# Kernel optimization log

Measured on AMD Instinct MI355X. Metric: run time of the kernel, lower is better.

The kernel has to match this reference:

```python
import jax, jax.numpy as jnp
import numpy as np

N = 100000      # nodes
E = 1600000     # edges (avg degree 16)
IN, HID, OUT = 128, 32, 64
H = 4           # attention heads in hidden layers

def _p(key, shape, scale=0.1):
    return jax.random.normal(key, shape, dtype=jnp.float32) * scale

def setup_inputs():
    key = jax.random.key(0)
    ks = jax.random.split(key, 16)
    return {
        "x": jax.random.normal(ks[0], (N, IN), dtype=jnp.float32),
        "edge_index": jax.random.randint(ks[1], (2, E), 0, N, dtype=jnp.int32),
        # layer 1: GATConv(IN -> HID, heads=4, concat=True) + BN
        "W1": _p(ks[2], (IN, H * HID)), "as1": _p(ks[3], (H, HID)), "ad1": _p(ks[4], (H, HID)),
        "b1": jnp.zeros((H * HID,), jnp.float32),
        "g1": jnp.ones((H * HID,), jnp.float32), "be1": jnp.zeros((H * HID,), jnp.float32),
        "rm1": _p(ks[5], (H * HID,)), "rv1": jnp.ones((H * HID,), jnp.float32),
        # layer 2: GATConv(H*HID -> HID, heads=4, concat=True) + BN
        "W2": _p(ks[6], (H * HID, H * HID)), "as2": _p(ks[7], (H, HID)), "ad2": _p(ks[8], (H, HID)),
        "b2": jnp.zeros((H * HID,), jnp.float32),
        "g2": jnp.ones((H * HID,), jnp.float32), "be2": jnp.zeros((H * HID,), jnp.float32),
        "rm2": _p(ks[9], (H * HID,)), "rv2": jnp.ones((H * HID,), jnp.float32),
        # layer 3: GATConv(H*HID -> OUT, heads=1, concat=False)
        "W3": _p(ks[10], (H * HID, OUT)), "as3": _p(ks[11], (1, OUT)), "ad3": _p(ks[12], (1, OUT)),
        "b3": jnp.zeros((OUT,), jnp.float32),
    }

def _gat(x, W, a_s, a_d, b, src, dst, heads, ch, concat):
    n = x.shape[0]
    h = (x @ W).reshape(n, heads, ch)                        # [N,H,C]
    e = (h * a_s).sum(-1)[src] + (h * a_d).sum(-1)[dst]      # per-edge logits [E,H]
    e = jax.nn.leaky_relu(e, 0.2)
    m = jax.ops.segment_max(e, dst, num_segments=n)          # segment softmax over dst
    ex = jnp.exp(e - m[dst])
    den = jax.ops.segment_sum(ex, dst, num_segments=n)
    alpha = ex / den[dst]                                    # self loops guarantee den > 0
    out = jax.ops.segment_sum(h[src] * alpha[:, :, None], dst, num_segments=n)
    out = out.reshape(n, heads * ch) if concat else out.mean(axis=1)
    return out + b

def _bn(x, g, b, rm, rv):                                    # BatchNorm1d, eval mode
    return (x - rm) * jax.lax.rsqrt(rv + 1e-5) * g + b

def _forward(x, edge_index, W1, as1, ad1, b1, g1, be1, rm1, rv1,
             W2, as2, ad2, b2, g2, be2, rm2, rv2, W3, as3, ad3, b3):
    n = x.shape[0]
    loop = jnp.arange(n, dtype=edge_index.dtype)             # add self loops (PyG default)
    src = jnp.concatenate([edge_index[0], loop])
    dst = jnp.concatenate([edge_index[1], loop])
    h = _gat(x, W1, as1, ad1, b1, src, dst, H, HID, True)
    h = jax.nn.elu(_bn(h, g1, be1, rm1, rv1))                # dropout = identity (eval)
    h = _gat(h, W2, as2, ad2, b2, src, dst, H, HID, True)
    h = jax.nn.elu(_bn(h, g2, be2, rm2, rv2))
    return _gat(h, W3, as3, ad3, b3, src, dst, 1, OUT, False)

def reference(x, edge_index, W1, as1, ad1, b1, g1, be1, rm1, rv1,
              W2, as2, ad2, b2, g2, be2, rm2, rv2, W3, as3, ad3, b3):
    return _forward(x, edge_index, W1, as1, ad1, b1, g1, be1, rm1, rv1,
                    W2, as2, ad2, b2, g2, be2, rm2, rv2, W3, as3, ad3, b3)
```

## Files before the change

### kernel.cpp

```cpp
#include <hip/hip_runtime.h>
#include <hip/hip_fp16.h>
#include <type_traits>

#define CDIV(a,b) (((a)+(b)-1)/(b))

typedef _Float16 f16x8 __attribute__((ext_vector_type(8)));
typedef float f32x4 __attribute__((ext_vector_type(4)));

__device__ __forceinline__ void wxform(const float* __restrict__ W,
                                       _Float16* __restrict__ Wt, int i, int NOUT) {
  int k = i / NOUT, c = i % NOUT;
  int s = k >> 5, g = (k >> 3) & 3, e = k & 7;
  Wt[(size_t)((s * 4 + g) * NOUT + c) * 8 + e] = (_Float16)W[i];
}
__global__ __launch_bounds__(256) void wprep_all(const float* __restrict__ W1,
                                                 const float* __restrict__ W2,
                                                 const float* __restrict__ W3,
                                                 _Float16* __restrict__ Wt1,
                                                 _Float16* __restrict__ Wt2,
                                                 _Float16* __restrict__ Wt3) {
  int i = blockIdx.x * blockDim.x + threadIdx.x;
  if (i < 128 * 128) { wxform(W1, Wt1, i, 128); wxform(W2, Wt2, i, 128); }
  if (i < 128 * 64)  { wxform(W3, Wt3, i, 64); }
}

template<typename AT>
__device__ __forceinline__ f16x8 load_afrag(const AT* __restrict__ xrow) {
  if constexpr (std::is_same<AT, _Float16>::value) {
    return *reinterpret_cast<const f16x8*>(xrow);
  } else {
    float4 v0 = *reinterpret_cast<const float4*>(xrow);
    float4 v1 = *reinterpret_cast<const float4*>(xrow + 4);
    f16x8 r = {(_Float16)v0.x, (_Float16)v0.y, (_Float16)v0.z, (_Float16)v0.w,
               (_Float16)v1.x, (_Float16)v1.y, (_Float16)v1.z, (_Float16)v1.w};
    return r;
  }
}

template<int NOUT, int HEADS, typename AT>
__global__ __launch_bounds__(256) void gemm_sc(const AT* __restrict__ X,
                                               const _Float16* __restrict__ Wt,
                                               const float* __restrict__ as_,
                                               const float* __restrict__ ad_,
                                               __half* __restrict__ Y,
                                               float* __restrict__ ssrc,
                                               float* __restrict__ sdst, int nrows) {
  constexpr int K = 128;
  constexpr int CT = NOUT / 16;
  constexpr int CH = NOUT / HEADS;
  constexpr int CPH = CH / 16;
  const int wave = threadIdx.x >> 6, lane = threadIdx.x & 63;
  const int g = lane >> 4, r16 = lane & 15;
  const int rt = blockIdx.x * 4 + wave;
  if (rt * 16 >= nrows) return;

  const AT* xrow = X + (size_t)(rt * 16 + r16) * K + g * 8;
  f16x8 a[4];
  #pragma unroll
  for (int s = 0; s < 4; ++s) a[s] = load_afrag(xrow + s * 32);

  f32x4 acc[CT];
  #pragma unroll
  for (int ct = 0; ct < CT; ++ct) acc[ct] = (f32x4){0.f, 0.f, 0.f, 0.f};

  #pragma unroll
  for (int ct = 0; ct < CT; ++ct) {
    #pragma unroll
    for (int s = 0; s < 4; ++s) {
      f16x8 b = *reinterpret_cast<const f16x8*>(&Wt[(size_t)((s * 4 + g) * NOUT + ct * 16 + r16) * 8]);
      acc[ct] = __builtin_amdgcn_mfma_f32_16x16x32_f16(a[s], b, acc[ct], 0, 0, 0);
    }
  }
  const int row0 = rt * 16 + g * 4;
  #pragma unroll
  for (int ct = 0; ct < CT; ++ct) {
    #pragma unroll
    for (int r = 0; r < 4; ++r) {
      Y[(size_t)(row0 + r) * NOUT + ct * 16 + r16] = __float2half_rn(acc[ct][r]);
    }
  }

  float pas[4][HEADS], pad_[4][HEADS];
  #pragma unroll
  for (int r = 0; r < 4; ++r)
    #pragma unroll
    for (int h = 0; h < HEADS; ++h) { pas[r][h] = 0.f; pad_[r][h] = 0.f; }
  #pragma unroll
  for (int h = 0; h < HEADS; ++h) {
    #pragma unroll
    for (int q = 0; q < CPH; ++q) {
      float asv = as_[h * CH + q * 16 + r16];
      float adv = ad_[h * CH + q * 16 + r16];
      #pragma unroll
      for (int r = 0; r < 4; ++r) {
        float av = acc[h * CPH + q][r];
        pas[r][h] += av * asv;
        pad_[r][h] += av * adv;
      }
    }
  }
  #pragma unroll
  for (int off = 1; off < 16; off <<= 1) {
    #pragma unroll
    for (int r = 0; r < 4; ++r)
      #pragma unroll
      for (int h = 0; h < HEADS; ++h) {
        pas[r][h] += __shfl_xor(pas[r][h], off);
        pad_[r][h] += __shfl_xor(pad_[r][h], off);
      }
  }
  #pragma unroll
  for (int h = 0; h < HEADS; ++h) {
    if (r16 == h) {
      #pragma unroll
      for (int r = 0; r < 4; ++r) ssrc[(size_t)(row0 + r) * HEADS + h] = pas[r][h];
    }
    if (r16 == 8 + h) {
      #pragma unroll
      for (int r = 0; r < 4; ++r) sdst[(size_t)(row0 + r) * HEADS + h] = pad_[r][h];
    }
  }
}

__global__ __launch_bounds__(256) void hist_kernel(const int* __restrict__ ei, int E,
                                                   int* __restrict__ deg) {
  int e = blockIdx.x * blockDim.x + threadIdx.x;
  if (e >= E) return;
  atomicAdd(&deg[ei[E + e]], 1);
}

__global__ __launch_bounds__(256) void scan_blocksums(const int* __restrict__ deg,
                                                      int* __restrict__ bsum, int N) {
  __shared__ int red[256];
  int base = blockIdx.x * 1024 + threadIdx.x * 4;
  int s = 0;
  #pragma unroll
  for (int i = 0; i < 4; ++i) { int idx = base + i; if (idx < N) s += deg[idx]; }
  red[threadIdx.x] = s;
  __syncthreads();
  for (int off = 128; off > 0; off >>= 1) {
    if (threadIdx.x < off) red[threadIdx.x] += red[threadIdx.x + off];
    __syncthreads();
  }
  if (threadIdx.x == 0) bsum[blockIdx.x] = red[0];
}

__global__ __launch_bounds__(1024) void scan_bsum(int* __restrict__ bsum, int nb) {
  __shared__ int sh[1024];
  int t = threadIdx.x;
  int v = (t < nb) ? bsum[t] : 0;
  sh[t] = v;
  __syncthreads();
  for (int off = 1; off < 1024; off <<= 1) {
    int tmp = (t >= off) ? sh[t - off] : 0;
    __syncthreads();
    sh[t] += tmp;
    __syncthreads();
  }
  if (t < nb) bsum[t] = sh[t] - v;
}

__global__ __launch_bounds__(256) void scan_final(const int* __restrict__ deg,
                                                  const int* __restrict__ bsum,
                                                  int* __restrict__ rowptr,
                                                  int* __restrict__ cursor, int N) {
  __shared__ int sh[256];
  const int t = threadIdx.x;
  const int base = blockIdx.x * 1024 + t * 4;
  int d[4] = {0, 0, 0, 0};
  #pragma unroll
  for (int i = 0; i < 4; ++i) if (base + i < N) d[i] = deg[base + i];
  int s = d[0] + d[1] + d[2] + d[3];
  sh[t] = s;
  __syncthreads();
  for (int off = 1; off < 256; off <<= 1) {
    int tmp = (t >= off) ? sh[t - off] : 0;
    __syncthreads();
    sh[t] += tmp;
    __syncthreads();
  }
  int run = bsum[blockIdx.x] + sh[t] - s;
  #pragma unroll
  for (int i = 0; i < 4; ++i) {
    if (base + i < N) { rowptr[base + i] = run; cursor[base + i] = run; run += d[i]; }
  }
  if (blockIdx.x == gridDim.x - 1 && t == 255) rowptr[N] = run;
}

__global__ __launch_bounds__(256) void scatter_pass(const int* __restrict__ ei, int E, int N,
                                                    int pw,
                                                    int* __restrict__ cursor,
                                                    int* __restrict__ col) {
  int e = blockIdx.x * blockDim.x + threadIdx.x;
  if (e >= E) return;
  int lo = blockIdx.y * pw;
  int hi = lo + pw;
  int d = ei[E + e];
  if (d < lo || d >= hi) return;
  int pos = atomicAdd(&cursor[d], 1);
  col[pos] = ei[e];
}

template<int HEADS, int CH, bool BN, bool OUTH>
__global__ __launch_bounds__(256) void gat_fused(
    const int* __restrict__ rowptr, const int* __restrict__ col,
    const __half* __restrict__ Hf,
    const float* __restrict__ ssrc, const float* __restrict__ sdst,
    const float* __restrict__ bias, const float* __restrict__ g,
    const float* __restrict__ be, const float* __restrict__ rm,
    const float* __restrict__ rv,
    void* __restrict__ outp, int N) {
  constexpr int NOUT = HEADS * CH;
  constexpr int VEC = NOUT / 64;
  constexpr int SLOTS = 64 / HEADS;
  __shared__ float ptile[4][SLOTS][HEADS];
  __shared__ int   stile[4][SLOTS];
  const int wv = threadIdx.x >> 6, lane = threadIdx.x & 63;
  const int n = blockIdx.x * 4 + wv;
  if (n >= N) return;
  const int eslot = lane / HEADS, head = lane & (HEADS - 1);
  const float sd = sdst[n * HEADS + head];
  float lgs = ssrc[n * HEADS + head] + sd;
  lgs = lgs > 0.f ? lgs : 0.2f * lgs;

  const int c0 = lane * VEC;
  const int hb = c0 / CH;

  float a0, a1 = 0.f;
  if (VEC == 2) {
    float2 hf = __half22float2(*reinterpret_cast<const __half2*>(&Hf[(size_t)n * NOUT + c0]));
    a0 = hf.x; a1 = hf.y;
  } else {
    a0 = __half2float(Hf[(size_t)n * NOUT + c0]);
  }

  float s = 0.f;
  const int beg = rowptr[n], end = rowptr[n + 1];
  for (int base = beg; base < end; base += SLOTS) {
    int e = base + eslot;
    float p = 0.f; int src = 0;
    if (e < end) {
      src = col[e];
      float lg = ssrc[src * HEADS + head] + sd;
      lg = lg > 0.f ? lg : 0.2f * lg;
      p = __expf(lg - lgs);
    }
    ptile[wv][eslot][head] = p;
    if (head == 0) stile[wv][eslot] = src;
    s += p;
    asm volatile("s_waitcnt lgkmcnt(0)" ::: "memory");

    int cnt = min(SLOTS, end - base);
    if (cnt == SLOTS) {
      #pragma unroll 16
      for (int j = 0; j < SLOTS; ++j) {
        int sj = stile[wv][j];
        float pj = ptile[wv][j][hb];
        if (VEC == 2) {
          float2 hf = __half22float2(*reinterpret_cast<const __half2*>(&Hf[(size_t)sj * NOUT + c0]));
          a0 += pj * hf.x; a1 += pj * hf.y;
        } else {
          a0 += pj * __half2float(Hf[(size_t)sj * NOUT + c0]);
        }
      }
    } else {
      for (int j = 0; j < cnt; ++j) {
        int sj = stile[wv][j];
        float pj = ptile[wv][j][hb];
        if (VEC == 2) {
          float2 hf = __half22float2(*reinterpret_cast<const __half2*>(&Hf[(size_t)sj * NOUT + c0]));
          a0 += pj * hf.x; a1 += pj * hf.y;
        } else {
          a0 += pj * __half2float(Hf[(size_t)sj * NOUT + c0]);
        }
      }
    }
  }

  #pragma unroll
  for (int off = HEADS; off < 64; off <<= 1) s += __shfl_xor(s, off);
  float inv = 1.f / (s + 1.f);
  float invb = __shfl(inv, hb);

  float o0 = a0 * invb + bias[c0];
  if (BN) {
    o0 = (o0 - rm[c0]) * rsqrtf(rv[c0] + 1e-5f) * g[c0] + be[c0];
    o0 = o0 > 0.f ? o0 : expm1f(o0);
  }
  if (VEC == 2) {
    float o1 = a1 * invb + bias[c0 + 1];
    if (BN) {
      o1 = (o1 - rm[c0 + 1]) * rsqrtf(rv[c0 + 1] + 1e-5f) * g[c0 + 1] + be[c0 + 1];
      o1 = o1 > 0.f ? o1 : expm1f(o1);
    }
    if (OUTH) {
      __half2 o = __floats2half2_rn(o0, o1);
      *reinterpret_cast<__half2*>(&((__half*)outp)[(size_t)n * NOUT + c0]) = o;
    } else {
      float2 o = make_float2(o0, o1);
      *reinterpret_cast<float2*>(&((float*)outp)[(size_t)n * NOUT + c0]) = o;
    }
  } else {
    if (OUTH) ((__half*)outp)[(size_t)n * NOUT + c0] = __float2half_rn(o0);
    else      ((float*)outp)[(size_t)n * NOUT + c0] = o0;
  }
}

extern "C" void kernel_launch(void* const* d_in, const int* in_sizes, int n_in,
                              void* d_out, int out_size, void* d_ws, size_t ws_size,
                              hipStream_t stream) {
  const float* x   = (const float*)d_in[0];
  const int*   ei  = (const int*)d_in[1];
  const float* W1  = (const float*)d_in[2];
  const float* as1 = (const float*)d_in[3];
  const float* ad1 = (const float*)d_in[4];
  const float* b1  = (const float*)d_in[5];
  const float* g1  = (const float*)d_in[6];
  const float* be1 = (const float*)d_in[7];
  const float* rm1 = (const float*)d_in[8];
  const float* rv1 = (const float*)d_in[9];
  const float* W2  = (const float*)d_in[10];
  const float* as2 = (const float*)d_in[11];
  const float* ad2 = (const float*)d_in[12];
  const float* b2  = (const float*)d_in[13];
  const float* g2  = (const float*)d_in[14];
  const float* be2 = (const float*)d_in[15];
  const float* rm2 = (const float*)d_in[16];
  const float* rv2 = (const float*)d_in[17];
  const float* W3  = (const float*)d_in[18];
  const float* as3 = (const float*)d_in[19];
  const float* ad3 = (const float*)d_in[20];
  const float* b3  = (const float*)d_in[21];

  const int N = in_sizes[0] / 128;
  const int E = in_sizes[1] / 2;
  float* out = (float*)d_out;

  char* p = (char*)d_ws;
  __half* Ah  = (__half*)p;  p += (size_t)N * 128 * 2;
  __half* Bh  = (__half*)p;  p += (size_t)N * 128 * 2;
  float* ssrc = (float*)p;   p += (size_t)N * 4 * 4;
  float* sdst = (float*)p;   p += (size_t)N * 4 * 4;
  int* deg    = (int*)p;     p += (size_t)N * 4;
  int* rowptr = (int*)p;     p += (size_t)(N + 1) * 4;
  int* cursor = (int*)p;     p += (size_t)N * 4;
  int* col    = (int*)p;     p += (size_t)E * 4;
  int* bsum   = (int*)p;     p += 4096;
  _Float16* Wt1 = (_Float16*)p; p += (size_t)128 * 128 * 2;
  _Float16* Wt2 = (_Float16*)p; p += (size_t)128 * 128 * 2;
  _Float16* Wt3 = (_Float16*)p;

  const int fusedB = CDIV(N, 4);
  const int nb = CDIV(N, 1024);
  const int gemmB = CDIV(N, 64);
  constexpr int NPASS = 8;
  const int pw = CDIV(N, NPASS);

  hipMemsetAsync(deg, 0, (size_t)N * sizeof(int), stream);
  hist_kernel<<<CDIV(E, 256), 256, 0, stream>>>(ei, E, deg);
  scan_blocksums<<<nb, 256, 0, stream>>>(deg, bsum, N);
  scan_bsum<<<1, 1024, 0, stream>>>(bsum, nb);
  scan_final<<<nb, 256, 0, stream>>>(deg, bsum, rowptr, cursor, N);
  scatter_pass<<<dim3(CDIV(E, 256), NPASS), 256, 0, stream>>>(ei, E, N, pw, cursor, col);

  wprep_all<<<CDIV(128 * 128, 256), 256, 0, stream>>>(W1, W2, W3, Wt1, Wt2, Wt3);

  gemm_sc<128, 4, float><<<gemmB, 256, 0, stream>>>(x, Wt1, as1, ad1, Ah, ssrc, sdst, N);
  gat_fused<4, 32, true, true><<<fusedB, 256, 0, stream>>>(rowptr, col, Ah, ssrc, sdst,
                                                           b1, g1, be1, rm1, rv1, Bh, N);

  gemm_sc<128, 4, _Float16><<<gemmB, 256, 0, stream>>>((const _Float16*)Bh, Wt2, as2, ad2,
                                                       Ah, ssrc, sdst, N);
  gat_fused<4, 32, true, true><<<fusedB, 256, 0, stream>>>(rowptr, col, Ah, ssrc, sdst,
                                                           b2, g2, be2, rm2, rv2, Bh, N);

  gemm_sc<64, 1, _Float16><<<gemmB, 256, 0, stream>>>((const _Float16*)Bh, Wt3, as3, ad3,
                                                      Ah, ssrc, sdst, N);
  gat_fused<1, 64, false, false><<<fusedB, 256, 0, stream>>>(rowptr, col, Ah, ssrc, sdst,
                                                             b3, b3, b3, b3, b3, out, N);
}
```

Measured before the change: 448.8 us.

## Split GAT aggregation into per-edge alpha pass and channel-sliced gather kernel

The GEMM now writes features in a 16-channel planar layout. The fused attention kernel is split in two. The first pass computes unnormalized per-edge attention weights as fp16 planes plus per-node inverse denominators. The second pass gathers one 16-channel slice per block using those stored weights. The aim is a smaller gather working set per slice and simpler inner loops. The cost is extra global traffic: alpha is written and re-read, col and alpha are re-read once per slice, and each gather is only 32 bytes wide.

Result: slower. 1.275 ms (+184.1%).

```diff
diff --git a/kernel.cpp b/kernel.cpp
--- a/kernel.cpp
+++ b/kernel.cpp
@@ -42,7 +42,7 @@
                                                const _Float16* __restrict__ Wt,
                                                const float* __restrict__ as_,
                                                const float* __restrict__ ad_,
-                                               __half* __restrict__ Y,
+                                               _Float16* __restrict__ Y,
                                                float* __restrict__ ssrc,
                                                float* __restrict__ sdst, int nrows) {
   constexpr int K = 128;
@@ -76,7 +76,7 @@
   for (int ct = 0; ct < CT; ++ct) {
     #pragma unroll
     for (int r = 0; r < 4; ++r) {
-      Y[(size_t)(row0 + r) * NOUT + ct * 16 + r16] = __float2half_rn(acc[ct][r]);
+      Y[((size_t)ct * nrows + row0 + r) * 16 + r16] = (_Float16)acc[ct][r];
     }
   }
 
@@ -201,20 +201,13 @@
   col[pos] = ei[e];
 }
 
-template<int HEADS, int CH, bool BN, bool OUTH>
-__global__ __launch_bounds__(256) void gat_fused(
+template<int HEADS>
+__global__ __launch_bounds__(256) void alpha_plane(
     const int* __restrict__ rowptr, const int* __restrict__ col,
-    const __half* __restrict__ Hf,
     const float* __restrict__ ssrc, const float* __restrict__ sdst,
-    const float* __restrict__ bias, const float* __restrict__ g,
-    const float* __restrict__ be, const float* __restrict__ rm,
-    const float* __restrict__ rv,
-    void* __restrict__ outp, int N) {
-  constexpr int NOUT = HEADS * CH;
-  constexpr int VEC = NOUT / 64;
+    _Float16* __restrict__ palpha, float* __restrict__ sinv,
+    int N, int E) {
   constexpr int SLOTS = 64 / HEADS;
-  __shared__ float ptile[4][SLOTS][HEADS];
-  __shared__ int   stile[4][SLOTS];
   const int wv = threadIdx.x >> 6, lane = threadIdx.x & 63;
   const int n = blockIdx.x * 4 + wv;
   if (n >= N) return;
@@ -222,87 +215,79 @@
   const float sd = sdst[n * HEADS + head];
   float lgs = ssrc[n * HEADS + head] + sd;
   lgs = lgs > 0.f ? lgs : 0.2f * lgs;
-
-  const int c0 = lane * VEC;
-  const int hb = c0 / CH;
-
-  float a0, a1 = 0.f;
-  if (VEC == 2) {
-    float2 hf = __half22float2(*reinterpret_cast<const __half2*>(&Hf[(size_t)n * NOUT + c0]));
-    a0 = hf.x; a1 = hf.y;
-  } else {
-    a0 = __half2float(Hf[(size_t)n * NOUT + c0]);
-  }
-
+  const size_t hp = (size_t)head * E;
   float s = 0.f;
   const int beg = rowptr[n], end = rowptr[n + 1];
   for (int base = beg; base < end; base += SLOTS) {
     int e = base + eslot;
-    float p = 0.f; int src = 0;
     if (e < end) {
-      src = col[e];
+      int src = col[e];
       float lg = ssrc[src * HEADS + head] + sd;
       lg = lg > 0.f ? lg : 0.2f * lg;
-      p = __expf(lg - lgs);
-    }
-    ptile[wv][eslot][head] = p;
-    if (head == 0) stile[wv][eslot] = src;
-    s += p;
-    asm volatile("s_waitcnt lgkmcnt(0)" ::: "memory");
-
-    int cnt = min(SLOTS, end - base);
-    if (cnt == SLOTS) {
-      #pragma unroll 16
-      for (int j = 0; j < SLOTS; ++j) {
-        int sj = stile[wv][j];
-        float pj = ptile[wv][j][hb];
-        if (VEC == 2) {
-          float2 hf = __half22float2(*reinterpret_cast<const __half2*>(&Hf[(size_t)sj * NOUT + c0]));
-          a0 += pj * hf.x; a1 += pj * hf.y;
-        } else {
-          a0 += pj * __half2float(Hf[(size_t)sj * NOUT + c0]);
-        }
-      }
-    } else {
-      for (int j = 0; j < cnt; ++j) {
-        int sj = stile[wv][j];
-        float pj = ptile[wv][j][hb];
-        if (VEC == 2) {
-          float2 hf = __half22float2(*reinterpret_cast<const __half2*>(&Hf[(size_t)sj * NOUT + c0]));
-          a0 += pj * hf.x; a1 += pj * hf.y;
-        } else {
-          a0 += pj * __half2float(Hf[(size_t)sj * NOUT + c0]);
-        }
-      }
-    }
-  }
-
+      float p = __expf(lg - lgs);
+      __builtin_nontemporal_store((_Float16)p, &palpha[hp + e]);
+      s += p;
+    }
+  }
   #pragma unroll
   for (int off = HEADS; off < 64; off <<= 1) s += __shfl_xor(s, off);
-  float inv = 1.f / (s + 1.f);
-  float invb = __shfl(inv, hb);
-
-  float o0 = a0 * invb + bias[c0];
-  if (BN) {
-    o0 = (o0 - rm[c0]) * rsqrtf(rv[c0] + 1e-5f) * g[c0] + be[c0];
-    o0 = o0 > 0.f ? o0 : expm1f(o0);
-  }
-  if (VEC == 2) {
-    float o1 = a1 * invb + bias[c0 + 1];
+  if (eslot == 0) sinv[n * HEADS + head] = 1.f / (s + 1.f);
+}
+
+template<int NOUT, int HEADS, int NSLICE, bool BN, bool OUTH>
+__global__ __launch_bounds__(256) void gat_slice(
+    const int* __restrict__ rowptr, const int* __restrict__ col,
+    const _Float16* __restrict__ Hf,
+    const _Float16* __restrict__ palpha, const float* __restrict__ sinv,
+    const float* __restrict__ bias, const float* __restrict__ g,
+    const float* __restrict__ be, const float* __restrict__ rm,
+    const float* __restrict__ rv,
+    void* __restrict__ outp, int N, int E) {
+  constexpr int CH = NOUT / HEADS;
+  const int slice = blockIdx.x % NSLICE;
+  const int chunk = blockIdx.x / NSLICE;
+  const int wv = threadIdx.x >> 6, lane = threadIdx.x & 63;
+  const int c = lane & 15, j = lane >> 4;
+  const int c0 = slice * 16 + c;
+  const int head = c0 / CH;
+  const size_t hplane = (size_t)head * E;
+  const _Float16* __restrict__ hpl = Hf + (size_t)slice * N * 16;
+  const int node0 = chunk * 64 + wv * 16;
+
+  for (int nn = 0; nn < 16; ++nn) {
+    const int n = node0 + nn;
+    if (n >= N) return;
+    const int beg = rowptr[n], end = rowptr[n + 1];
+    float a = (j == 0) ? (float)hpl[(size_t)n * 16 + c] : 0.f;
+    float a2 = 0.f;
+    for (int base = beg; base < end; base += 8) {
+      int e1 = base + j, e2 = base + 4 + j;
+      bool v1 = e1 < end, v2 = e2 < end;
+      int ec1 = v1 ? e1 : beg, ec2 = v2 ? e2 : beg;
+      int s1 = __builtin_nontemporal_load(&col[ec1]);
+      int s2 = __builtin_nontemporal_load(&col[ec2]);
+      float p1 = (float)__builtin_nontemporal_load(&palpha[hplane + ec1]);
+      float p2 = (float)__builtin_nontemporal_load(&palpha[hplane + ec2]);
+      p1 = v1 ? p1 : 0.f;
+      p2 = v2 ? p2 : 0.f;
+      float h1 = (float)hpl[(size_t)s1 * 16 + c];
+      float h2 = (float)hpl[(size_t)s2 * 16 + c];
+      a  += p1 * h1;
+      a2 += p2 * h2;
+    }
+    a += a2;
+    a += __shfl_xor(a, 16);
+    a += __shfl_xor(a, 32);
+    float inv = sinv[n * HEADS + head];
+    float o = a * inv + bias[c0];
     if (BN) {
-      o1 = (o1 - rm[c0 + 1]) * rsqrtf(rv[c0 + 1] + 1e-5f) * g[c0 + 1] + be[c0 + 1];
-      o1 = o1 > 0.f ? o1 : expm1f(o1);
-    }
-    if (OUTH) {
-      __half2 o = __floats2half2_rn(o0, o1);
-      *reinterpret_cast<__half2*>(&((__half*)outp)[(size_t)n * NOUT + c0]) = o;
-    } else {
-      float2 o = make_float2(o0, o1);
-      *reinterpret_cast<float2*>(&((float*)outp)[(size_t)n * NOUT + c0]) = o;
-    }
-  } else {
-    if (OUTH) ((__half*)outp)[(size_t)n * NOUT + c0] = __float2half_rn(o0);
-    else      ((float*)outp)[(size_t)n * NOUT + c0] = o0;
+      o = (o - rm[c0]) * rsqrtf(rv[c0] + 1e-5f) * g[c0] + be[c0];
+      o = o > 0.f ? o : expm1f(o);
+    }
+    if (lane < 16) {
+      if (OUTH) ((__half*)outp)[(size_t)n * NOUT + c0] = __float2half_rn(o);
+      else      ((float*)outp)[(size_t)n * NOUT + c0] = o;
+    }
   }
 }
 
@@ -337,10 +322,12 @@
   float* out = (float*)d_out;
 
   char* p = (char*)d_ws;
-  __half* Ah  = (__half*)p;  p += (size_t)N * 128 * 2;
-  __half* Bh  = (__half*)p;  p += (size_t)N * 128 * 2;
+  _Float16* Ah  = (_Float16*)p;  p += (size_t)N * 128 * 2;
+  __half* Bh    = (__half*)p;    p += (size_t)N * 128 * 2;
   float* ssrc = (float*)p;   p += (size_t)N * 4 * 4;
   float* sdst = (float*)p;   p += (size_t)N * 4 * 4;
+  float* sinv = (float*)p;   p += (size_t)N * 4 * 4;
+  _Float16* palpha = (_Float16*)p; p += (size_t)E * 4 * 2;
   int* deg    = (int*)p;     p += (size_t)N * 4;
   int* rowptr = (int*)p;     p += (size_t)(N + 1) * 4;
   int* cursor = (int*)p;     p += (size_t)N * 4;
@@ -350,9 +337,11 @@
   _Float16* Wt2 = (_Float16*)p; p += (size_t)128 * 128 * 2;
   _Float16* Wt3 = (_Float16*)p;
 
-  const int fusedB = CDIV(N, 4);
+  const int alphaB = CDIV(N, 4);
   const int nb = CDIV(N, 1024);
   const int gemmB = CDIV(N, 64);
+  const int sliceB8 = 8 * CDIV(N, 64);
+  const int sliceB4 = 4 * CDIV(N, 64);
   constexpr int NPASS = 8;
   const int pw = CDIV(N, NPASS);
 
@@ -366,16 +355,19 @@
   wprep_all<<<CDIV(128 * 128, 256), 256, 0, stream>>>(W1, W2, W3, Wt1, Wt2, Wt3);
 
   gemm_sc<128, 4, float><<<gemmB, 256, 0, stream>>>(x, Wt1, as1, ad1, Ah, ssrc, sdst, N);
-  gat_fused<4, 32, true, true><<<fusedB, 256, 0, stream>>>(rowptr, col, Ah, ssrc, sdst,
-                                                           b1, g1, be1, rm1, rv1, Bh, N);
+  alpha_plane<4><<<alphaB, 256, 0, stream>>>(rowptr, col, ssrc, sdst, palpha, sinv, N, E);
+  gat_slice<128, 4, 8, true, true><<<sliceB8, 256, 0, stream>>>(rowptr, col, Ah, palpha, sinv,
+                                                                b1, g1, be1, rm1, rv1, Bh, N, E);
 
   gemm_sc<128, 4, _Float16><<<gemmB, 256, 0, stream>>>((const _Float16*)Bh, Wt2, as2, ad2,
                                                        Ah, ssrc, sdst, N);
-  gat_fused<4, 32, true, true><<<fusedB, 256, 0, stream>>>(rowptr, col, Ah, ssrc, sdst,
-                                                           b2, g2, be2, rm2, rv2, Bh, N);
+  alpha_plane<4><<<alphaB, 256, 0, stream>>>(rowptr, col, ssrc, sdst, palpha, sinv, N, E);
+  gat_slice<128, 4, 8, true, true><<<sliceB8, 256, 0, stream>>>(rowptr, col, Ah, palpha, sinv,
+                                                                b2, g2, be2, rm2, rv2, Bh, N, E);
 
   gemm_sc<64, 1, _Float16><<<gemmB, 256, 0, stream>>>((const _Float16*)Bh, Wt3, as3, ad3,
                                                       Ah, ssrc, sdst, N);
-  gat_fused<1, 64, false, false><<<fusedB, 256, 0, stream>>>(rowptr, col, Ah, ssrc, sdst,
-                                                             b3, b3, b3, b3, b3, out, N);
-}
+  alpha_plane<1><<<alphaB, 256, 0, stream>>>(rowptr, col, ssrc, sdst, palpha, sinv, N, E);
+  gat_slice<64, 1, 4, false, false><<<sliceB4, 256, 0, stream>>>(rowptr, col, Ah, palpha, sinv,
+                                                                 b3, b3, b3, b3, b3, out, N, E);
+}
```
